# Optimization experiments

Measured on AMD Instinct MI355X. Metric: run time of the kernel, lower is better.

Reference implementation:

```python
import jax, jax.numpy as jnp
import numpy as np

NUM_HEAD, DIM_HEAD, IN_DIM = 16, 64, 1024
SLEN, BSZ = 2048, 8


def elu_p1_sum_norm_eps(x):
    # F.elu(x,1.0)+1 == where(x>0, x+1, exp(x)); then normalize over last dim
    y = jnp.where(x > 0, x + 1.0, jnp.exp(x))
    return y / (y.sum(-1, keepdims=True) + 1e-5)


def setup_inputs() -> dict:
    key = jax.random.key(0)
    ks = jax.random.split(key, 4)
    x = jax.random.normal(ks[0], (SLEN, BSZ, IN_DIM), dtype=jnp.float32)
    state = jnp.zeros((BSZ, NUM_HEAD, DIM_HEAD, DIM_HEAD), dtype=jnp.float32)
    # nn.Linear weights: [out_features, in_features]
    W_qkv = jax.random.normal(ks[1], (NUM_HEAD * 3 * DIM_HEAD, IN_DIM), dtype=jnp.float32) / np.sqrt(IN_DIM)
    W_out = jax.random.normal(ks[2], (IN_DIM, NUM_HEAD * DIM_HEAD), dtype=jnp.float32) / np.sqrt(NUM_HEAD * DIM_HEAD)
    ln_gamma = jnp.ones((IN_DIM,), dtype=jnp.float32)
    ln_beta = jnp.zeros((IN_DIM,), dtype=jnp.float32)
    return {"x": x, "state": state, "W_qkv": W_qkv, "W_out": W_out,
            "ln_gamma": ln_gamma, "ln_beta": ln_beta}


def reference(x, state, W_qkv, W_out, ln_gamma, ln_beta):
    slen, bsz, _ = x.shape
    # LayerNorm
    mu = x.mean(-1, keepdims=True)
    var = ((x - mu) ** 2).mean(-1, keepdims=True)
    h = (x - mu) / jnp.sqrt(var + 1e-5) * ln_gamma + ln_beta
    # slow net -> q,k,v  [S,B,H,3D]
    qkv = jnp.einsum('sbi,oi->sbo', h, W_qkv).reshape(slen, bsz, NUM_HEAD, 3 * DIM_HEAD)
    q, k, v = jnp.split(qkv, 3, axis=-1)  # each [S,B,H,D]
    q = elu_p1_sum_norm_eps(q)
    k = elu_p1_sum_norm_eps(k)

    # fast-weight sum recurrence: W_t = W_{t-1} + k_t (x) v_t ; o_t = q_t W_t
    def step(W, qkv_t):
        q_t, k_t, v_t = qkv_t  # [B,H,D]
        W = W + k_t[..., :, None] * v_t[..., None, :]  # [B,H,D,D]
        o_t = jnp.einsum('bhd,bhde->bhe', q_t, W)
        return W, o_t

    W_final, outs = jax.lax.scan(step, state, (q, k, v))  # outs [S,B,H,D]
    out = outs.reshape(slen, bsz, NUM_HEAD * DIM_HEAD)
    out = jnp.einsum('sbj,ij->sbi', out, W_out)
    # dropout p=0 (eval) -> identity
    return x + out, W_final
```

## Files before the change

kernel.cpp:

```cpp
#include <hip/hip_runtime.h>

typedef unsigned short u16;
typedef __attribute__((ext_vector_type(4))) unsigned short u16x4;
typedef __attribute__((ext_vector_type(8))) unsigned short u16x8;
typedef __attribute__((ext_vector_type(8))) __bf16 bf16x8;
typedef __attribute__((ext_vector_type(4))) float f32x4;

#define SLEN_ 2048
#define BSZ_ 8
#define NH_ 16
#define DH_ 64
#define IND_ 1024
#define MROWS_ (SLEN_*BSZ_)
#define NQKV_ (NH_*3*DH_)
#define NOUT_ (NH_*DH_)
#define NT_ 16

__device__ __forceinline__ float b2f(u16 u) {
    return __uint_as_float(((unsigned)u) << 16);
}
__device__ __forceinline__ u16 f2b(float f) {
    unsigned u = __float_as_uint(f);
    u = u + 0x7FFFu + ((u >> 16) & 1u);
    return (u16)(u >> 16);
}

#define GLOAD_LDS16(g, l) __builtin_amdgcn_global_load_lds( \
    (const __attribute__((address_space(1))) unsigned int*)(g), \
    (__attribute__((address_space(3))) unsigned int*)(l), 16, 0, 0)

#define TI(r, c) ((((r) << 7) + ((c) << 1)) ^ (((r) & 7) << 4))

__global__ __launch_bounds__(256) void cast_weights(
        const float* __restrict__ wq, const float* __restrict__ wo,
        u16* __restrict__ wqb, u16* __restrict__ wob)
{
    int i = blockIdx.x * 256 + threadIdx.x;
    const int NQ4 = NQKV_ * IND_ / 4;
    float4 v;
    u16* dst;
    if (i < NQ4) { v = ((const float4*)wq)[i]; dst = wqb + (size_t)i * 4; }
    else { int j = i - NQ4; v = ((const float4*)wo)[j]; dst = wob + (size_t)j * 4; }
    u16x4 o;
    o[0] = f2b(v.x); o[1] = f2b(v.y); o[2] = f2b(v.z); o[3] = f2b(v.w);
    *(u16x4*)dst = o;
}

__global__ __launch_bounds__(256) void ln_kernel(
        const float* __restrict__ x, const float* __restrict__ g,
        const float* __restrict__ bt, u16* __restrict__ h)
{
    int row = blockIdx.x, tid = threadIdx.x;
    const float4 v = ((const float4*)(x + (size_t)row * IND_))[tid];
    float s  = v.x + v.y + v.z + v.w;
    float s2 = v.x*v.x + v.y*v.y + v.z*v.z + v.w*v.w;
    #pragma unroll
    for (int m = 1; m < 64; m <<= 1) { s += __shfl_xor(s, m); s2 += __shfl_xor(s2, m); }
    __shared__ float sh[8];
    int w = tid >> 6, l = tid & 63;
    if (l == 0) { sh[w] = s; sh[4 + w] = s2; }
    __syncthreads();
    s  = sh[0] + sh[1] + sh[2] + sh[3];
    s2 = sh[4] + sh[5] + sh[6] + sh[7];
    float mu   = s * (1.f / IND_);
    float var  = s2 * (1.f / IND_) - mu * mu;
    float rstd = rsqrtf(var + 1e-5f);
    float4 gg = ((const float4*)g)[tid];
    float4 bb = ((const float4*)bt)[tid];
    u16x4 o;
    o[0] = f2b((v.x - mu) * rstd * gg.x + bb.x);
    o[1] = f2b((v.y - mu) * rstd * gg.y + bb.y);
    o[2] = f2b((v.z - mu) * rstd * gg.z + bb.z);
    o[3] = f2b((v.w - mu) * rstd * gg.w + bb.w);
    ((u16x4*)(h + (size_t)row * IND_))[tid] = o;
}

template<int MODE>
__global__ __launch_bounds__(512, 2) void gemm256(
        const u16* __restrict__ A, const u16* __restrict__ Bm,
        u16* __restrict__ Cb, float* __restrict__ Cf, const float* __restrict__ X,
        int M, int N, int K)
{
    __shared__ char smem[131072];

    const int tid = threadIdx.x;
    const int w = tid >> 6, l = tid & 63;
    const int wmi = w >> 2, wni = w & 3;
    const int fr = l & 15, fq = l >> 4;

    const int h = blockIdx.y * gridDim.x + blockIdx.x;
    const int xcd = h & 7, i = h >> 3;
    const int bm = xcd * 8 + (i & 7);
    const int bn = i >> 3;

    const int sr = l >> 3;
    const int sc = ((l & 7) ^ sr) * 8;
    const u16* ga = A  + (size_t)(bm * 256 + w * 8 + sr) * K + sc;
    const u16* gb = Bm + (size_t)(bn * 256 + w * 8 + sr) * K + sc;
    char* lA = smem + w * 1024;
    char* lB = smem + 32768 + w * 1024;
    const size_t K64 = (size_t)K * 64;

#define STAGE(t, bufb) { \
    const u16* gat = ga + (t) * 64; const u16* gbt = gb + (t) * 64; \
    char* la = lA + (bufb) * 65536; char* lb = lB + (bufb) * 65536; \
    GLOAD_LDS16(gat,            la);            \
    GLOAD_LDS16(gat + K64,      la + 8192);     \
    GLOAD_LDS16(gat + 2 * K64,  la + 16384);    \
    GLOAD_LDS16(gat + 3 * K64,  la + 24576);    \
    GLOAD_LDS16(gbt,            lb);            \
    GLOAD_LDS16(gbt + K64,      lb + 8192);     \
    GLOAD_LDS16(gbt + 2 * K64,  lb + 16384);    \
    GLOAD_LDS16(gbt + 3 * K64,  lb + 24576);    \
}

    const int cswz = (fr & 7) << 4;
    const int c0 = (fq * 16) ^ cswz;
    const int c1 = (64 + fq * 16) ^ cswz;
    const char* rdA = smem + (wmi * 128 + fr) * 128;
    const char* rdB = smem + 32768 + (wni * 64 + fr) * 128;

#define RD_FRAGS(dstA, dstB, base_off, cc) { \
    const char* bA_ = rdA + (base_off); const char* bB_ = rdB + (base_off); \
    _Pragma("unroll") for (int m_ = 0; m_ < 8; m_++) \
        dstA[m_] = *(const bf16x8*)(bA_ + m_ * 2048 + (cc)); \
    _Pragma("unroll") for (int n_ = 0; n_ < 4; n_++) \
        dstB[n_] = *(const bf16x8*)(bB_ + n_ * 2048 + (cc)); \
}

#define MFMA32(srcA, srcB) { \
    _Pragma("unroll") for (int m_ = 0; m_ < 8; m_++) \
        _Pragma("unroll") for (int n_ = 0; n_ < 4; n_++) \
            acc[m_][n_] = __builtin_amdgcn_mfma_f32_16x16x32_bf16(srcA[m_], srcB[n_], acc[m_][n_], 0, 0, 0); \
}

    f32x4 acc[8][4] = {};
    bf16x8 fsA_A[8], fsA_B[4];
    bf16x8 fsB_A[8], fsB_B[4];

    STAGE(0, 0);
    STAGE(1, 1);
    asm volatile("s_waitcnt vmcnt(8)" ::: "memory");
    __builtin_amdgcn_s_barrier();
    RD_FRAGS(fsA_A, fsA_B, 0, c0);
    asm volatile("s_waitcnt lgkmcnt(0)" ::: "memory");
    __builtin_amdgcn_sched_barrier(0);

    #pragma unroll 1
    for (int t = 0; t < NT_; t++) {
        const int cur = (t & 1) * 65536;
        const int nxt = ((t + 1) & 1) * 65536;
        RD_FRAGS(fsB_A, fsB_B, cur, c1);
        __builtin_amdgcn_s_setprio(1);
        MFMA32(fsA_A, fsA_B);
        __builtin_amdgcn_s_setprio(0);
        asm volatile("s_waitcnt lgkmcnt(0)" ::: "memory");
        __builtin_amdgcn_sched_barrier(0);
        __builtin_amdgcn_s_barrier();
        if (t + 2 < NT_) STAGE(t + 2, t & 1);
        if (t < NT_ - 2) asm volatile("s_waitcnt vmcnt(8)" ::: "memory");
        else             asm volatile("s_waitcnt vmcnt(0)" ::: "memory");
        __builtin_amdgcn_s_barrier();
        if (t < NT_ - 1) RD_FRAGS(fsA_A, fsA_B, nxt, c0);
        __builtin_amdgcn_s_setprio(1);
        MFMA32(fsB_A, fsB_B);
        __builtin_amdgcn_s_setprio(0);
        asm volatile("s_waitcnt lgkmcnt(0)" ::: "memory");
        __builtin_amdgcn_sched_barrier(0);
        __builtin_amdgcn_s_barrier();
    }
#undef STAGE
#undef RD_FRAGS
#undef MFMA32

    #pragma unroll
    for (int m = 0; m < 8; m++)
        #pragma unroll
        for (int r = 0; r < 4; r++) {
            int row = bm * 256 + wmi * 128 + m * 16 + fq * 4 + r;
            #pragma unroll
            for (int n = 0; n < 4; n++) {
                int col = bn * 256 + wni * 64 + n * 16 + fr;
                float vv = acc[m][n][r];
                if (MODE == 0) {
                    Cb[(size_t)row * N + col] = f2b(vv);
                } else {
                    size_t idx = (size_t)row * N + col;
                    Cf[idx] = vv + X[idx];
                }
            }
        }
}

__global__ __launch_bounds__(256) void scan2(
        const u16* __restrict__ qkv, const float* __restrict__ state,
        u16* __restrict__ obf, float* __restrict__ wfin)
{
    __shared__ u16 Q_l[4096], K_l[4096], Kt_l[4096], Vt_l[4096], P_l[4096], W_l[4096];

    const int bh = blockIdx.x;
    const int b = bh >> 4, hh = bh & 15;
    const int tid = threadIdx.x;
    const int w = tid >> 6, l = tid & 63;
    const int fr = l & 15, fq = l >> 4;

    f32x4 accW[4];
    #pragma unroll
    for (int jt = 0; jt < 4; jt++) {
        #pragma unroll
        for (int r = 0; r < 4; r++) {
            int d = jt * 16 + fr, e = w * 16 + fq * 4 + r;
            float sv = state[(size_t)bh * 4096 + d * 64 + e];
            accW[jt][r] = sv;
            *(u16*)((char*)W_l + TI(e, d)) = f2b(sv);
        }
    }

    int goff = (w == 0) ? 0 : (w == 1) ? 64 : (w == 2) ? 128 : 160;
    const u16* g0 = qkv + ((size_t)l * BSZ_ + b) * NQKV_ + hh * 192 + goff;
    const size_t chunk_stride = (size_t)64 * BSZ_ * NQKV_;

    u16x8 pre[8];
    if (w < 2) {
        #pragma unroll
        for (int j = 0; j < 8; j++) pre[j] = *(const u16x8*)(g0 + j * 8);
    } else {
        #pragma unroll
        for (int j = 0; j < 4; j++) pre[j] = *(const u16x8*)(g0 + j * 8);
    }

    __syncthreads();

    #pragma unroll 1
    for (int n = 0; n < 32; n++) {
        if (w < 2) {
            float f[64];
            #pragma unroll
            for (int j = 0; j < 8; j++)
                #pragma unroll
                for (int m = 0; m < 8; m++) {
                    float x = b2f(pre[j][m]);
                    f[j * 8 + m] = x > 0.f ? x + 1.f : __expf(x);
                }
            float s = 0.f;
            #pragma unroll
            for (int i = 0; i < 64; i++) s += f[i];
            float inv = 1.f / (s + 1e-5f);
            u16* dst = (w == 0) ? Q_l : K_l;
            #pragma unroll
            for (int j = 0; j < 8; j++) {
                u16x8 o;
                #pragma unroll
                for (int m = 0; m < 8; m++) o[m] = f2b(f[j * 8 + m] * inv);
                *(u16x8*)((char*)dst + TI(l, j * 8)) = o;
                if (w == 1) {
                    #pragma unroll
                    for (int m = 0; m < 8; m++)
                        *(u16*)((char*)Kt_l + TI(j * 8 + m, l)) = o[m];
                }
            }
        } else {
            int e0 = (w == 2) ? 0 : 32;
            #pragma unroll
            for (int j = 0; j < 4; j++)
                #pragma unroll
                for (int m = 0; m < 8; m++)
                    *(u16*)((char*)Vt_l + TI(e0 + j * 8 + m, l)) = pre[j][m];
        }
        __syncthreads();

        if (n < 31) {
            const u16* gn = g0 + (size_t)(n + 1) * chunk_stride;
            if (w < 2) {
                #pragma unroll
                for (int j = 0; j < 8; j++) pre[j] = *(const u16x8*)(gn + j * 8);
            } else {
                #pragma unroll
                for (int j = 0; j < 4; j++) pre[j] = *(const u16x8*)(gn + j * 8);
            }
        }

        f32x4 aS[4] = {};
        bf16x8 aK[2];
        #pragma unroll
        for (int ks = 0; ks < 2; ks++)
            aK[ks] = *(const bf16x8*)((const char*)K_l + TI(w * 16 + fr, ks * 32 + fq * 8));
        #pragma unroll
        for (int jt = 0; jt < 4; jt++)
            #pragma unroll
            for (int ks = 0; ks < 2; ks++) {
                bf16x8 bq = *(const bf16x8*)((const char*)Q_l + TI(jt * 16 + fr, ks * 32 + fq * 8));
                aS[jt] = __builtin_amdgcn_mfma_f32_16x16x32_bf16(aK[ks], bq, aS[jt], 0, 0, 0);
            }
        #pragma unroll
        for (int jt = 0; jt < 4; jt++) {
            int t = jt * 16 + fr;
            int s0 = w * 16 + fq * 4;
            unsigned pk0, pk1;
            {
                u16 e0 = (s0 + 0 <= t) ? f2b(aS[jt][0]) : (u16)0;
                u16 e1 = (s0 + 1 <= t) ? f2b(aS[jt][1]) : (u16)0;
                u16 e2 = (s0 + 2 <= t) ? f2b(aS[jt][2]) : (u16)0;
                u16 e3 = (s0 + 3 <= t) ? f2b(aS[jt][3]) : (u16)0;
                pk0 = (unsigned)e0 | ((unsigned)e1 << 16);
                pk1 = (unsigned)e2 | ((unsigned)e3 << 16);
            }
            uint2 pkk; pkk.x = pk0; pkk.y = pk1;
            *(uint2*)((char*)P_l + TI(t, s0)) = pkk;
        }
        __syncthreads();

        f32x4 aO[4] = {};
        bf16x8 ap[2], aq2[2], av[2];
        #pragma unroll
        for (int ks = 0; ks < 2; ks++) {
            ap[ks]  = *(const bf16x8*)((const char*)P_l  + TI(w * 16 + fr, ks * 32 + fq * 8));
            aq2[ks] = *(const bf16x8*)((const char*)Q_l  + TI(w * 16 + fr, ks * 32 + fq * 8));
            av[ks]  = *(const bf16x8*)((const char*)Vt_l + TI(w * 16 + fr, ks * 32 + fq * 8));
        }
        #pragma unroll
        for (int jt = 0; jt < 4; jt++) {
            #pragma unroll
            for (int ks = 0; ks < 2; ks++) {
                bf16x8 bv = *(const bf16x8*)((const char*)Vt_l + TI(jt * 16 + fr, ks * 32 + fq * 8));
                aO[jt] = __builtin_amdgcn_mfma_f32_16x16x32_bf16(ap[ks], bv, aO[jt], 0, 0, 0);
            }
            #pragma unroll
            for (int ks = 0; ks < 2; ks++) {
                bf16x8 bw = *(const bf16x8*)((const char*)W_l + TI(jt * 16 + fr, ks * 32 + fq * 8));
                aO[jt] = __builtin_amdgcn_mfma_f32_16x16x32_bf16(aq2[ks], bw, aO[jt], 0, 0, 0);
            }
            #pragma unroll
            for (int ks = 0; ks < 2; ks++) {
                bf16x8 bk = *(const bf16x8*)((const char*)Kt_l + TI(jt * 16 + fr, ks * 32 + fq * 8));
                accW[jt] = __builtin_amdgcn_mfma_f32_16x16x32_bf16(av[ks], bk, accW[jt], 0, 0, 0);
            }
        }
        __syncthreads();

        #pragma unroll
        for (int jt = 0; jt < 4; jt++)
            #pragma unroll
            for (int r = 0; r < 4; r++) {
                int e = w * 16 + fq * 4 + r, d = jt * 16 + fr;
                *(u16*)((char*)W_l + TI(e, d)) = f2b(accW[jt][r]);
                *(u16*)((char*)P_l + TI(e, d)) = f2b(aO[jt][r]);
            }
        __syncthreads();

        {
            int t = tid >> 2, seg = tid & 3;
            u16x8 o1 = *(const u16x8*)((const char*)P_l + TI(t, seg * 16));
            u16x8 o2 = *(const u16x8*)((const char*)P_l + TI(t, seg * 16 + 8));
            u16* gd = obf + ((size_t)(n * 64 + t) * BSZ_ + b) * NOUT_ + hh * 64 + seg * 16;
            *(u16x8*)(gd) = o1;
            *(u16x8*)(gd + 8) = o2;
        }
    }

    #pragma unroll
    for (int jt = 0; jt < 4; jt++)
        #pragma unroll
        for (int r = 0; r < 4; r++) {
            int d = jt * 16 + fr, e = w * 16 + fq * 4 + r;
            wfin[(size_t)bh * 4096 + d * 64 + e] = accW[jt][r];
        }
}

extern "C" void kernel_launch(void* const* d_in, const int* in_sizes, int n_in,
                              void* d_out, int out_size, void* d_ws, size_t ws_size,
                              hipStream_t stream) {
    const float* x     = (const float*)d_in[0];
    const float* state = (const float*)d_in[1];
    const float* wqkv  = (const float*)d_in[2];
    const float* wout  = (const float*)d_in[3];
    const float* gamma = (const float*)d_in[4];
    const float* beta  = (const float*)d_in[5];

    float* out0 = (float*)d_out;
    float* wfin = (float*)d_out + (size_t)MROWS_ * IND_;

    char* ws = (char*)d_ws;
    u16* qkv_bf = (u16*)ws;
    u16* h_bf   = (u16*)(ws + 100663296);
    u16* o_bf   = h_bf;
    u16* wq_bf  = (u16*)(ws + 100663296 + 33554432);
    u16* wo_bf  = (u16*)(ws + 100663296 + 33554432 + 6291456);

    cast_weights<<<4096, 256, 0, stream>>>(wqkv, wout, wq_bf, wo_bf);
    ln_kernel<<<MROWS_, 256, 0, stream>>>(x, gamma, beta, h_bf);
    dim3 g1(MROWS_ / 256, NQKV_ / 256);
    gemm256<0><<<g1, 512, 0, stream>>>(h_bf, wq_bf, qkv_bf, nullptr, nullptr, MROWS_, NQKV_, IND_);
    scan2<<<128, 256, 0, stream>>>(qkv_bf, state, o_bf, wfin);
    dim3 g2(MROWS_ / 256, NOUT_ / 256);
    gemm256<1><<<g2, 512, 0, stream>>>(o_bf, wo_bf, nullptr, out0, x, MROWS_, NOUT_, IND_);
}
```

Before: 300.3 us.

## Split sequential chunk scan into parallel intra-chunk, prefix, and inter-chunk kernels

Replaces the single 128-block scan kernel, which walks 32 chunks in sequence, with three kernels. The first computes the intra-chunk causal output and each chunk's K^T V state delta in parallel across all 4096 chunk blocks. The second takes a prefix sum over the chunk deltas to get each chunk's starting state and the final state. The third adds q times the starting state to the output. This exposes far more parallelism than 128 blocks on a large GPU, at the cost of extra global traffic for per-chunk states, a read-modify-write of the output, and extra bf16 rounding of the states.

```diff
diff --git a/kernel.cpp b/kernel.cpp
--- a/kernel.cpp
+++ b/kernel.cpp
@@ -192,33 +192,20 @@
         }
 }
 
-__global__ __launch_bounds__(256) void scan2(
-        const u16* __restrict__ qkv, const float* __restrict__ state,
-        u16* __restrict__ obf, float* __restrict__ wfin)
-{
-    __shared__ u16 Q_l[4096], K_l[4096], Kt_l[4096], Vt_l[4096], P_l[4096], W_l[4096];
-
-    const int bh = blockIdx.x;
+__global__ __launch_bounds__(256) void scanA(
+        const u16* __restrict__ qkv, u16* __restrict__ obf, u16* __restrict__ Sbuf)
+{
+    __shared__ u16 Q_l[4096], K_l[4096], Kt_l[4096], Vt_l[4096], P_l[4096];
+
+    const int blk = blockIdx.x;
+    const int bh = blk & 127, n = blk >> 7;
     const int b = bh >> 4, hh = bh & 15;
     const int tid = threadIdx.x;
     const int w = tid >> 6, l = tid & 63;
     const int fr = l & 15, fq = l >> 4;
 
-    f32x4 accW[4];
-    #pragma unroll
-    for (int jt = 0; jt < 4; jt++) {
-        #pragma unroll
-        for (int r = 0; r < 4; r++) {
-            int d = jt * 16 + fr, e = w * 16 + fq * 4 + r;
-            float sv = state[(size_t)bh * 4096 + d * 64 + e];
-            accW[jt][r] = sv;
-            *(u16*)((char*)W_l + TI(e, d)) = f2b(sv);
-        }
-    }
-
     int goff = (w == 0) ? 0 : (w == 1) ? 64 : (w == 2) ? 128 : 160;
-    const u16* g0 = qkv + ((size_t)l * BSZ_ + b) * NQKV_ + hh * 192 + goff;
-    const size_t chunk_stride = (size_t)64 * BSZ_ * NQKV_;
+    const u16* g0 = qkv + ((size_t)(n * 64 + l) * BSZ_ + b) * NQKV_ + hh * 192 + goff;
 
     u16x8 pre[8];
     if (w < 2) {
@@ -229,142 +216,218 @@
         for (int j = 0; j < 4; j++) pre[j] = *(const u16x8*)(g0 + j * 8);
     }
 
-    __syncthreads();
-
-    #pragma unroll 1
-    for (int n = 0; n < 32; n++) {
-        if (w < 2) {
-            float f[64];
-            #pragma unroll
-            for (int j = 0; j < 8; j++)
-                #pragma unroll
-                for (int m = 0; m < 8; m++) {
-                    float x = b2f(pre[j][m]);
-                    f[j * 8 + m] = x > 0.f ? x + 1.f : __expf(x);
-                }
-            float s = 0.f;
-            #pragma unroll
-            for (int i = 0; i < 64; i++) s += f[i];
-            float inv = 1.f / (s + 1e-5f);
-            u16* dst = (w == 0) ? Q_l : K_l;
-            #pragma unroll
-            for (int j = 0; j < 8; j++) {
-                u16x8 o;
-                #pragma unroll
-                for (int m = 0; m < 8; m++) o[m] = f2b(f[j * 8 + m] * inv);
-                *(u16x8*)((char*)dst + TI(l, j * 8)) = o;
-                if (w == 1) {
-                    #pragma unroll
-                    for (int m = 0; m < 8; m++)
-                        *(u16*)((char*)Kt_l + TI(j * 8 + m, l)) = o[m];
-                }
+    if (w < 2) {
+        float f[64];
+        #pragma unroll
+        for (int j = 0; j < 8; j++)
+            #pragma unroll
+            for (int m = 0; m < 8; m++) {
+                float x = b2f(pre[j][m]);
+                f[j * 8 + m] = x > 0.f ? x + 1.f : __expf(x);
             }
-        } else {
-            int e0 = (w == 2) ? 0 : 32;
-            #pragma unroll
-            for (int j = 0; j < 4; j++)
+        float s = 0.f;
+        #pragma unroll
+        for (int i = 0; i < 64; i++) s += f[i];
+        float inv = 1.f / (s + 1e-5f);
+        u16* dst = (w == 0) ? Q_l : K_l;
+        #pragma unroll
+        for (int j = 0; j < 8; j++) {
+            u16x8 o;
+            #pragma unroll
+            for (int m = 0; m < 8; m++) o[m] = f2b(f[j * 8 + m] * inv);
+            *(u16x8*)((char*)dst + TI(l, j * 8)) = o;
+            if (w == 1) {
                 #pragma unroll
                 for (int m = 0; m < 8; m++)
-                    *(u16*)((char*)Vt_l + TI(e0 + j * 8 + m, l)) = pre[j][m];
-        }
-        __syncthreads();
-
-        if (n < 31) {
-            const u16* gn = g0 + (size_t)(n + 1) * chunk_stride;
-            if (w < 2) {
-                #pragma unroll
-                for (int j = 0; j < 8; j++) pre[j] = *(const u16x8*)(gn + j * 8);
-            } else {
-                #pragma unroll
-                for (int j = 0; j < 4; j++) pre[j] = *(const u16x8*)(gn + j * 8);
+                    *(u16*)((char*)Kt_l + TI(j * 8 + m, l)) = o[m];
             }
         }
-
-        f32x4 aS[4] = {};
-        bf16x8 aK[2];
-        #pragma unroll
-        for (int ks = 0; ks < 2; ks++)
-            aK[ks] = *(const bf16x8*)((const char*)K_l + TI(w * 16 + fr, ks * 32 + fq * 8));
-        #pragma unroll
-        for (int jt = 0; jt < 4; jt++)
-            #pragma unroll
-            for (int ks = 0; ks < 2; ks++) {
-                bf16x8 bq = *(const bf16x8*)((const char*)Q_l + TI(jt * 16 + fr, ks * 32 + fq * 8));
-                aS[jt] = __builtin_amdgcn_mfma_f32_16x16x32_bf16(aK[ks], bq, aS[jt], 0, 0, 0);
+    } else {
+        int e0 = (w == 2) ? 0 : 32;
+        #pragma unroll
+        for (int j = 0; j < 4; j++)
+            #pragma unroll
+            for (int m = 0; m < 8; m++)
+                *(u16*)((char*)Vt_l + TI(e0 + j * 8 + m, l)) = pre[j][m];
+    }
+    __syncthreads();
+
+    f32x4 aS[4] = {};
+    bf16x8 aK[2];
+    #pragma unroll
+    for (int ks = 0; ks < 2; ks++)
+        aK[ks] = *(const bf16x8*)((const char*)K_l + TI(w * 16 + fr, ks * 32 + fq * 8));
+    #pragma unroll
+    for (int jt = 0; jt < 4; jt++)
+        #pragma unroll
+        for (int ks = 0; ks < 2; ks++) {
+            bf16x8 bq = *(const bf16x8*)((const char*)Q_l + TI(jt * 16 + fr, ks * 32 + fq * 8));
+            aS[jt] = __builtin_amdgcn_mfma_f32_16x16x32_bf16(aK[ks], bq, aS[jt], 0, 0, 0);
+        }
+    #pragma unroll
+    for (int jt = 0; jt < 4; jt++) {
+        int t = jt * 16 + fr;
+        int s0 = w * 16 + fq * 4;
+        u16 e0 = (s0 + 0 <= t) ? f2b(aS[jt][0]) : (u16)0;
+        u16 e1 = (s0 + 1 <= t) ? f2b(aS[jt][1]) : (u16)0;
+        u16 e2 = (s0 + 2 <= t) ? f2b(aS[jt][2]) : (u16)0;
+        u16 e3 = (s0 + 3 <= t) ? f2b(aS[jt][3]) : (u16)0;
+        uint2 pkk;
+        pkk.x = (unsigned)e0 | ((unsigned)e1 << 16);
+        pkk.y = (unsigned)e2 | ((unsigned)e3 << 16);
+        *(uint2*)((char*)P_l + TI(t, s0)) = pkk;
+    }
+    __syncthreads();
+
+    f32x4 aO[4] = {}, aS2[4] = {};
+    bf16x8 ap[2], akt[2];
+    #pragma unroll
+    for (int ks = 0; ks < 2; ks++) {
+        ap[ks]  = *(const bf16x8*)((const char*)P_l  + TI(w * 16 + fr, ks * 32 + fq * 8));
+        akt[ks] = *(const bf16x8*)((const char*)Kt_l + TI(w * 16 + fr, ks * 32 + fq * 8));
+    }
+    #pragma unroll
+    for (int jt = 0; jt < 4; jt++) {
+        #pragma unroll
+        for (int ks = 0; ks < 2; ks++) {
+            bf16x8 bv = *(const bf16x8*)((const char*)Vt_l + TI(jt * 16 + fr, ks * 32 + fq * 8));
+            aO[jt]  = __builtin_amdgcn_mfma_f32_16x16x32_bf16(ap[ks],  bv, aO[jt],  0, 0, 0);
+            aS2[jt] = __builtin_amdgcn_mfma_f32_16x16x32_bf16(akt[ks], bv, aS2[jt], 0, 0, 0);
+        }
+    }
+    __syncthreads();
+
+    u16* Sg = Sbuf + ((size_t)bh * 32 + n) * 4096;
+    #pragma unroll
+    for (int jt = 0; jt < 4; jt++)
+        #pragma unroll
+        for (int r = 0; r < 4; r++) {
+            int rr = w * 16 + fq * 4 + r, cc = jt * 16 + fr;
+            *(u16*)((char*)P_l + TI(rr, cc)) = f2b(aO[jt][r]);
+            Sg[rr * 64 + cc] = f2b(aS2[jt][r]);
+        }
+    __syncthreads();
+
+    {
+        int t = tid >> 2, seg = tid & 3;
+        u16x8 o1 = *(const u16x8*)((const char*)P_l + TI(t, seg * 16));
+        u16x8 o2 = *(const u16x8*)((const char*)P_l + TI(t, seg * 16 + 8));
+        u16* gd = obf + ((size_t)(n * 64 + t) * BSZ_ + b) * NOUT_ + hh * 64 + seg * 16;
+        *(u16x8*)(gd) = o1;
+        *(u16x8*)(gd + 8) = o2;
+    }
+}
+
+__global__ __launch_bounds__(256) void scanB(
+        u16* __restrict__ Sbuf, const float* __restrict__ state, float* __restrict__ wfin)
+{
+    const int blk = blockIdx.x;
+    const int bh = blk >> 2;
+    const int e0 = (blk & 3) * 1024 + threadIdx.x * 4;
+    float4 acc = *(const float4*)(state + (size_t)bh * 4096 + e0);
+    u16* Sp = Sbuf + (size_t)bh * 32 * 4096 + e0;
+    #pragma unroll
+    for (int nn = 0; nn < 32; nn++) {
+        u16x4 s = *(const u16x4*)(Sp + nn * 4096);
+        u16x4 p;
+        p[0] = f2b(acc.x); p[1] = f2b(acc.y); p[2] = f2b(acc.z); p[3] = f2b(acc.w);
+        *(u16x4*)(Sp + nn * 4096) = p;
+        acc.x += b2f(s[0]); acc.y += b2f(s[1]);
+        acc.z += b2f(s[2]); acc.w += b2f(s[3]);
+    }
+    *(float4*)(wfin + (size_t)bh * 4096 + e0) = acc;
+}
+
+__global__ __launch_bounds__(256) void scanC(
+        const u16* __restrict__ qkv, const u16* __restrict__ Sbuf, u16* __restrict__ obf)
+{
+    __shared__ u16 Q_l[4096], W_l[4096];
+
+    const int blk = blockIdx.x;
+    const int bh = blk & 127, n = blk >> 7;
+    const int b = bh >> 4, hh = bh & 15;
+    const int tid = threadIdx.x;
+    const int w = tid >> 6, l = tid & 63;
+    const int fr = l & 15, fq = l >> 4;
+
+    const u16* g0 = qkv + ((size_t)(n * 64 + l) * BSZ_ + b) * NQKV_ + hh * 192;
+    u16x8 pre[8];
+    if (w == 0) {
+        #pragma unroll
+        for (int j = 0; j < 8; j++) pre[j] = *(const u16x8*)(g0 + j * 8);
+    }
+
+    const u16* Wp = Sbuf + ((size_t)bh * 32 + n) * 4096;
+    #pragma unroll
+    for (int k2 = 0; k2 < 4; k2++) {
+        int g = tid * 4 + k2 * 1024;
+        u16x4 s = *(const u16x4*)(Wp + g);
+        int d = g >> 6, e = g & 63;
+        #pragma unroll
+        for (int i2 = 0; i2 < 4; i2++)
+            *(u16*)((char*)W_l + TI(e + i2, d)) = s[i2];
+    }
+
+    if (w == 0) {
+        float f[64];
+        #pragma unroll
+        for (int j = 0; j < 8; j++)
+            #pragma unroll
+            for (int m = 0; m < 8; m++) {
+                float x = b2f(pre[j][m]);
+                f[j * 8 + m] = x > 0.f ? x + 1.f : __expf(x);
             }
-        #pragma unroll
-        for (int jt = 0; jt < 4; jt++) {
-            int t = jt * 16 + fr;
-            int s0 = w * 16 + fq * 4;
-            unsigned pk0, pk1;
-            {
-                u16 e0 = (s0 + 0 <= t) ? f2b(aS[jt][0]) : (u16)0;
-                u16 e1 = (s0 + 1 <= t) ? f2b(aS[jt][1]) : (u16)0;
-                u16 e2 = (s0 + 2 <= t) ? f2b(aS[jt][2]) : (u16)0;
-                u16 e3 = (s0 + 3 <= t) ? f2b(aS[jt][3]) : (u16)0;
-                pk0 = (unsigned)e0 | ((unsigned)e1 << 16);
-                pk1 = (unsigned)e2 | ((unsigned)e3 << 16);
-            }
-            uint2 pkk; pkk.x = pk0; pkk.y = pk1;
-            *(uint2*)((char*)P_l + TI(t, s0)) = pkk;
-        }
-        __syncthreads();
-
-        f32x4 aO[4] = {};
-        bf16x8 ap[2], aq2[2], av[2];
+        float s = 0.f;
+        #pragma unroll
+        for (int i = 0; i < 64; i++) s += f[i];
+        float inv = 1.f / (s + 1e-5f);
+        #pragma unroll
+        for (int j = 0; j < 8; j++) {
+            u16x8 o;
+            #pragma unroll
+            for (int m = 0; m < 8; m++) o[m] = f2b(f[j * 8 + m] * inv);
+            *(u16x8*)((char*)Q_l + TI(l, j * 8)) = o;
+        }
+    }
+    __syncthreads();
+
+    f32x4 aO[4] = {};
+    bf16x8 aq[2];
+    #pragma unroll
+    for (int ks = 0; ks < 2; ks++)
+        aq[ks] = *(const bf16x8*)((const char*)Q_l + TI(w * 16 + fr, ks * 32 + fq * 8));
+    #pragma unroll
+    for (int jt = 0; jt < 4; jt++)
         #pragma unroll
         for (int ks = 0; ks < 2; ks++) {
-            ap[ks]  = *(const bf16x8*)((const char*)P_l  + TI(w * 16 + fr, ks * 32 + fq * 8));
-            aq2[ks] = *(const bf16x8*)((const char*)Q_l  + TI(w * 16 + fr, ks * 32 + fq * 8));
-            av[ks]  = *(const bf16x8*)((const char*)Vt_l + TI(w * 16 + fr, ks * 32 + fq * 8));
-        }
-        #pragma unroll
-        for (int jt = 0; jt < 4; jt++) {
-            #pragma unroll
-            for (int ks = 0; ks < 2; ks++) {
-                bf16x8 bv = *(const bf16x8*)((const char*)Vt_l + TI(jt * 16 + fr, ks * 32 + fq * 8));
-                aO[jt] = __builtin_amdgcn_mfma_f32_16x16x32_bf16(ap[ks], bv, aO[jt], 0, 0, 0);
-            }
-            #pragma unroll
-            for (int ks = 0; ks < 2; ks++) {
-                bf16x8 bw = *(const bf16x8*)((const char*)W_l + TI(jt * 16 + fr, ks * 32 + fq * 8));
-                aO[jt] = __builtin_amdgcn_mfma_f32_16x16x32_bf16(aq2[ks], bw, aO[jt], 0, 0, 0);
-            }
-            #pragma unroll
-            for (int ks = 0; ks < 2; ks++) {
-                bf16x8 bk = *(const bf16x8*)((const char*)Kt_l + TI(jt * 16 + fr, ks * 32 + fq * 8));
-                accW[jt] = __builtin_amdgcn_mfma_f32_16x16x32_bf16(av[ks], bk, accW[jt], 0, 0, 0);
-            }
-        }
-        __syncthreads();
-
-        #pragma unroll
-        for (int jt = 0; jt < 4; jt++)
-            #pragma unroll
-            for (int r = 0; r < 4; r++) {
-                int e = w * 16 + fq * 4 + r, d = jt * 16 + fr;
-                *(u16*)((char*)W_l + TI(e, d)) = f2b(accW[jt][r]);
-                *(u16*)((char*)P_l + TI(e, d)) = f2b(aO[jt][r]);
-            }
-        __syncthreads();
-
-        {
-            int t = tid >> 2, seg = tid & 3;
-            u16x8 o1 = *(const u16x8*)((const char*)P_l + TI(t, seg * 16));
-            u16x8 o2 = *(const u16x8*)((const char*)P_l + TI(t, seg * 16 + 8));
-            u16* gd = obf + ((size_t)(n * 64 + t) * BSZ_ + b) * NOUT_ + hh * 64 + seg * 16;
-            *(u16x8*)(gd) = o1;
-            *(u16x8*)(gd + 8) = o2;
-        }
-    }
+            bf16x8 bw = *(const bf16x8*)((const char*)W_l + TI(jt * 16 + fr, ks * 32 + fq * 8));
+            aO[jt] = __builtin_amdgcn_mfma_f32_16x16x32_bf16(aq[ks], bw, aO[jt], 0, 0, 0);
+        }
+    __syncthreads();
 
     #pragma unroll
     for (int jt = 0; jt < 4; jt++)
         #pragma unroll
-        for (int r = 0; r < 4; r++) {
-            int d = jt * 16 + fr, e = w * 16 + fq * 4 + r;
-            wfin[(size_t)bh * 4096 + d * 64 + e] = accW[jt][r];
-        }
+        for (int r = 0; r < 4; r++)
+            *(u16*)((char*)W_l + TI(w * 16 + fq * 4 + r, jt * 16 + fr)) = f2b(aO[jt][r]);
+    __syncthreads();
+
+    {
+        int t = tid >> 2, seg = tid & 3;
+        u16* gd = obf + ((size_t)(n * 64 + t) * BSZ_ + b) * NOUT_ + hh * 64 + seg * 16;
+        u16x8 a1 = *(const u16x8*)((const char*)W_l + TI(t, seg * 16));
+        u16x8 a2 = *(const u16x8*)((const char*)W_l + TI(t, seg * 16 + 8));
+        u16x8 g1 = *(const u16x8*)(gd);
+        u16x8 g2 = *(const u16x8*)(gd + 8);
+        u16x8 r1, r2;
+        #pragma unroll
+        for (int m = 0; m < 8; m++) {
+            r1[m] = f2b(b2f(a1[m]) + b2f(g1[m]));
+            r2[m] = f2b(b2f(a2[m]) + b2f(g2[m]));
+        }
+        *(u16x8*)(gd) = r1;
+        *(u16x8*)(gd + 8) = r2;
+    }
 }
 
 extern "C" void kernel_launch(void* const* d_in, const int* in_sizes, int n_in,
@@ -384,14 +447,17 @@
     u16* qkv_bf = (u16*)ws;
     u16* h_bf   = (u16*)(ws + 100663296);
     u16* o_bf   = h_bf;
-    u16* wq_bf  = (u16*)(ws + 100663296 + 33554432);
-    u16* wo_bf  = (u16*)(ws + 100663296 + 33554432 + 6291456);
+    u16* wq_bf  = (u16*)(ws + 134217728);
+    u16* wo_bf  = (u16*)(ws + 140509184);
+    u16* S_bf   = (u16*)(ws + 142606336);
 
     cast_weights<<<4096, 256, 0, stream>>>(wqkv, wout, wq_bf, wo_bf);
     ln_kernel<<<MROWS_, 256, 0, stream>>>(x, gamma, beta, h_bf);
     dim3 g1(MROWS_ / 256, NQKV_ / 256);
     gemm256<0><<<g1, 512, 0, stream>>>(h_bf, wq_bf, qkv_bf, nullptr, nullptr, MROWS_, NQKV_, IND_);
-    scan2<<<128, 256, 0, stream>>>(qkv_bf, state, o_bf, wfin);
+    scanA<<<4096, 256, 0, stream>>>(qkv_bf, o_bf, S_bf);
+    scanB<<<512, 256, 0, stream>>>(S_bf, state, wfin);
+    scanC<<<4096, 256, 0, stream>>>(qkv_bf, S_bf, o_bf);
     dim3 g2(MROWS_ / 256, NOUT_ / 256);
     gemm256<1><<<g2, 512, 0, stream>>>(o_bf, wo_bf, nullptr, out0, x, MROWS_, NOUT_, IND_);
 }
```

Result: faster. 252.3 us (-16.0%).
